# Performance work log

Measured on AMD Instinct MI355X. Metric: run time of the kernel, lower is better.

The kernel has to match this reference:

```python
import jax, jax.numpy as jnp
import numpy as np

NREF, NALT, B, D, F = 131072, 32768, 4096, 128, 512
H = F // 2  # d_ffn // 2
EPS = 1e-5


def _ln(x, w, b):
    m = jnp.mean(x, axis=-1, keepdims=True)
    v = jnp.mean((x - m) ** 2, axis=-1, keepdims=True)
    return (x - m) * jax.lax.rsqrt(v + EPS) * w + b


def setup_inputs() -> dict:
    key = jax.random.key(0)
    ks = jax.random.split(key, 16)
    s = 0.02
    return {
        "ref_flat": jax.random.normal(ks[0], (NREF, D), jnp.float32),
        "alt_flat": jax.random.normal(ks[1], (NALT, D), jnp.float32),
        "ref_seg": jnp.sort(jax.random.randint(ks[2], (NREF,), 0, B)),
        "alt_seg": jnp.sort(jax.random.randint(ks[3], (NALT,), 0, B)),
        "norm1_w": jnp.ones((D,), jnp.float32),
        "norm1_b": jnp.zeros((D,), jnp.float32),
        "w1_ref": jax.random.normal(ks[4], (D, F), jnp.float32) * s,
        "b1_ref": jnp.zeros((F,), jnp.float32),
        "w1_alt": jax.random.normal(ks[5], (D, F), jnp.float32) * s,
        "b1_alt": jnp.zeros((F,), jnp.float32),
        "norm2_w": jnp.ones((H,), jnp.float32),
        "norm2_b": jnp.zeros((H,), jnp.float32),
        "alpha_ref": jnp.float32(0.01),
        "alpha_alt": jnp.float32(0.01),
        "beta_ref": jnp.float32(0.01),
        "beta_alt": jnp.float32(0.01),
        "gamma": jnp.float32(0.01),
        "ref_regularizer": 0.1 * jnp.ones((H,), jnp.float32),
        "reg_w_pre": jnp.float32(np.log(0.1)),
        "w2_ref": jax.random.normal(ks[6], (H, D), jnp.float32) * s,
        "b2_ref": jnp.zeros((D,), jnp.float32),
        "w2_alt": jax.random.normal(ks[7], (H, D), jnp.float32) * s,
        "b2_alt": jnp.zeros((D,), jnp.float32),
    }


def reference(ref_flat, alt_flat, ref_seg, alt_seg,
              norm1_w, norm1_b, w1_ref, b1_ref, w1_alt, b1_alt,
              norm2_w, norm2_b, alpha_ref, alpha_alt, beta_ref, beta_alt,
              gamma, ref_regularizer, reg_w_pre, w2_ref, b2_ref, w2_alt, b2_alt):
    # proj1 + SELU on flattened ragged reads
    zr = jax.nn.selu(_ln(ref_flat, norm1_w, norm1_b) @ w1_ref + b1_ref)   # [NREF, F]
    za = jax.nn.selu(_ln(alt_flat, norm1_w, norm1_b) @ w1_alt + b1_alt)   # [NALT, F]
    z1r, z2r = zr[:, :H], zr[:, H:]
    z1a, z2a = za[:, :H], za[:, H:]
    z2r = _ln(z2r, norm2_w, norm2_b)
    z2a = _ln(z2a, norm2_w, norm2_b)

    cnt_r = jax.ops.segment_sum(jnp.ones((NREF,), z2r.dtype), ref_seg, num_segments=B)
    cnt_a = jax.ops.segment_sum(jnp.ones((NALT,), z2a.dtype), alt_seg, num_segments=B)
    reg_w = jnp.exp(reg_w_pre) + 0.25
    # regularized mean field over each ref set
    ref_mf = (jax.ops.segment_sum(z2r, ref_seg, num_segments=B)
              + reg_w * ref_regularizer) / (cnt_r[:, None] + reg_w)       # [B, H]
    alt_mf = jax.ops.segment_sum(z2a, alt_seg, num_segments=B) \
             / jnp.maximum(cnt_a, 1.0)[:, None]                            # [B, H]

    ref_gate = z2r * alpha_ref + 1.0 + (beta_ref * ref_mf)[ref_seg]
    alt_gate = z2a * alpha_alt + 1.0 + (beta_alt * alt_mf + gamma * ref_mf)[alt_seg]

    out_r = ref_flat + (z1r * ref_gate) @ w2_ref + b2_ref
    out_a = alt_flat + (z1a * alt_gate) @ w2_alt + b2_alt
    return out_r, out_a
```

## Files before the change

### kernel.cpp

```cpp
#include <hip/hip_runtime.h>
#include <hip/hip_bf16.h>

#define NREF 131072
#define NALT 32768
#define BSEG 4096
#define D 128
#define F 512
#define H 256
#define EPS 1e-5f

typedef short short8 __attribute__((ext_vector_type(8)));
typedef float f32x4 __attribute__((ext_vector_type(4)));

__device__ __forceinline__ float selu_f(float z) {
    const float sc = 1.0507009873554805f;
    const float al = 1.6732632423543772f;
    return z > 0.f ? sc * z : sc * al * (__expf(z) - 1.f);
}

__device__ __forceinline__ short f2bf(float v) {
    __bf16 b = (__bf16)v;
    return __builtin_bit_cast(short, b);
}

__device__ __forceinline__ float bf2f(short s) {
    return (float)__builtin_bit_cast(__bf16, s);
}

__global__ void pack_w(const float* __restrict__ w, __bf16* __restrict__ wp, int KT, int N) {
    int idx = blockIdx.x * 256 + threadIdx.x;
    int j = idx & 7;
    int l = (idx >> 3) & 63;
    int t = idx >> 9;
    int kt = t % KT;
    int nt = t / KT;
    int k = kt * 32 + ((l >> 4) << 3) + j;
    int n = (nt << 4) + (l & 15);
    wp[idx] = (__bf16)w[k * N + n];
}

__global__ __launch_bounds__(256, 4)
void pass1_kernel(const float* __restrict__ x, const int* __restrict__ seg,
                  const __bf16* __restrict__ w1p, const float* __restrict__ b1,
                  const float* __restrict__ n1w, const float* __restrict__ n1b,
                  const float* __restrict__ n2w, const float* __restrict__ n2b,
                  float* __restrict__ seg_sum, float* __restrict__ seg_cnt,
                  __bf16* __restrict__ z2n_out) {
    __shared__ __align__(16) __bf16 ys[32 * 128];
    __shared__ __align__(16) __bf16 z2s[32 * 256];
    __shared__ float n2w_s[H], n2b_s[H];
    __shared__ int seg_s[32];

    const int tid = threadIdx.x;
    const int lane = tid & 63;
    const int wv = tid >> 6;
    const int q = lane >> 4, m0 = lane & 15;
    const size_t row0 = (size_t)blockIdx.x * 32;

    short8 bb[2][4];
    #pragma unroll
    for (int p = 0; p < 2; ++p)
        #pragma unroll
        for (int kt = 0; kt < 4; ++kt)
            bb[p][kt] = *reinterpret_cast<const short8*>(
                w1p + ((size_t)((16 + wv * 4 + p) * 4 + kt) * 64 + lane) * 8);
    float b1v[4];
    #pragma unroll
    for (int nt = 0; nt < 4; ++nt) b1v[nt] = b1[256 + (wv * 4 + nt) * 16 + m0];

    const int r = tid >> 3, g = tid & 7;
    float xr[16];
    #pragma unroll
    for (int i = 0; i < 4; ++i) {
        float4 t = *reinterpret_cast<const float4*>(x + (row0 + r) * D + g * 16 + i * 4);
        xr[i * 4 + 0] = t.x; xr[i * 4 + 1] = t.y; xr[i * 4 + 2] = t.z; xr[i * 4 + 3] = t.w;
    }
    float w1r[16], c1r[16];
    #pragma unroll
    for (int i = 0; i < 4; ++i) {
        float4 t = *reinterpret_cast<const float4*>(n1w + g * 16 + i * 4);
        w1r[i * 4 + 0] = t.x; w1r[i * 4 + 1] = t.y; w1r[i * 4 + 2] = t.z; w1r[i * 4 + 3] = t.w;
        float4 u = *reinterpret_cast<const float4*>(n1b + g * 16 + i * 4);
        c1r[i * 4 + 0] = u.x; c1r[i * 4 + 1] = u.y; c1r[i * 4 + 2] = u.z; c1r[i * 4 + 3] = u.w;
    }

    n2w_s[tid] = n2w[tid]; n2b_s[tid] = n2b[tid];
    if (tid < 32) seg_s[tid] = seg[row0 + tid];

    {
        float s = 0.f, ss = 0.f;
        #pragma unroll
        for (int i = 0; i < 16; ++i) { s += xr[i]; ss += xr[i] * xr[i]; }
        s += __shfl_xor(s, 1); ss += __shfl_xor(ss, 1);
        s += __shfl_xor(s, 2); ss += __shfl_xor(ss, 2);
        s += __shfl_xor(s, 4); ss += __shfl_xor(ss, 4);
        float mean = s * (1.f / 128.f);
        float var = ss * (1.f / 128.f) - mean * mean;
        float rsv = rsqrtf(var + EPS);
        const int swr = (r & 7) << 3;
        #pragma unroll
        for (int h = 0; h < 2; ++h) {
            short8 pk;
            #pragma unroll
            for (int j = 0; j < 8; ++j)
                pk[j] = f2bf((xr[h * 8 + j] - mean) * rsv * w1r[h * 8 + j] + c1r[h * 8 + j]);
            *reinterpret_cast<short8*>(&ys[r * 128 + ((g * 16 + h * 8) ^ swr)]) = pk;
        }
    }
    __syncthreads();

    {
        const int swm = (m0 & 7) << 3;
        const int ccol = q << 3;
        short8 a0[4], a1[4];
        #pragma unroll
        for (int kt = 0; kt < 4; ++kt) {
            a0[kt] = *reinterpret_cast<const short8*>(&ys[m0 * 128 + ((kt * 32 + ccol) ^ swm)]);
            a1[kt] = *reinterpret_cast<const short8*>(&ys[(m0 + 16) * 128 + ((kt * 32 + ccol) ^ swm)]);
        }
        #pragma unroll
        for (int nt = 0; nt < 4; ++nt) {
            f32x4 acc0 = {0.f, 0.f, 0.f, 0.f};
            f32x4 acc1 = {0.f, 0.f, 0.f, 0.f};
            #pragma unroll
            for (int kt = 0; kt < 4; ++kt) {
                acc0 = __builtin_amdgcn_mfma_f32_16x16x32_bf16(a0[kt], bb[nt & 1][kt], acc0, 0, 0, 0);
                acc1 = __builtin_amdgcn_mfma_f32_16x16x32_bf16(a1[kt], bb[nt & 1][kt], acc1, 0, 0, 0);
            }
            if (nt < 2) {
                #pragma unroll
                for (int kt = 0; kt < 4; ++kt)
                    bb[nt & 1][kt] = *reinterpret_cast<const short8*>(
                        w1p + ((size_t)((16 + wv * 4 + nt + 2) * 4 + kt) * 64 + lane) * 8);
            }
            int cz = (wv * 4 + nt) * 16 + m0;
            #pragma unroll
            for (int reg = 0; reg < 4; ++reg) {
                int r0 = (q << 2) + reg;
                int r1 = r0 + 16;
                z2s[r0 * 256 + (cz ^ ((r0 & 7) << 3))] = (__bf16)selu_f(acc0[reg] + b1v[nt]);
                z2s[r1 * 256 + (cz ^ ((r1 & 7) << 3))] = (__bf16)selu_f(acc1[reg] + b1v[nt]);
            }
        }
    }
    __syncthreads();

    {
        const int swr = (r & 7) << 3;
        float vb[32];
        float s2 = 0.f, q2 = 0.f;
        #pragma unroll
        for (int i = 0; i < 4; ++i) {
            short8 v = *reinterpret_cast<const short8*>(&z2s[r * 256 + ((g * 32 + i * 8) ^ swr)]);
            #pragma unroll
            for (int j = 0; j < 8; ++j) {
                float f = bf2f(v[j]);
                vb[i * 8 + j] = f; s2 += f; q2 += f * f;
            }
        }
        s2 += __shfl_xor(s2, 1); q2 += __shfl_xor(q2, 1);
        s2 += __shfl_xor(s2, 2); q2 += __shfl_xor(q2, 2);
        s2 += __shfl_xor(s2, 4); q2 += __shfl_xor(q2, 4);
        float mean2 = s2 * (1.f / 256.f);
        float var2 = q2 * (1.f / 256.f) - mean2 * mean2;
        float rs2 = rsqrtf(var2 + EPS);
        #pragma unroll
        for (int i = 0; i < 4; ++i) {
            short8 o;
            #pragma unroll
            for (int j = 0; j < 8; ++j) {
                int col = g * 32 + i * 8 + j;
                o[j] = f2bf((vb[i * 8 + j] - mean2) * rs2 * n2w_s[col] + n2b_s[col]);
            }
            *reinterpret_cast<short8*>(&z2s[r * 256 + ((g * 32 + i * 8) ^ swr)]) = o;
            *reinterpret_cast<short8*>(z2n_out + (row0 + r) * H + g * 32 + i * 8) = o;
        }
    }
    __syncthreads();

    {
        int c = tid;
        int s_cur = seg_s[0];
        float run = 0.f;
        for (int rr = 0; rr < 32; ++rr) {
            int sg = seg_s[rr];
            if (sg != s_cur) {
                atomicAdd(&seg_sum[(size_t)s_cur * H + c], run);
                run = 0.f; s_cur = sg;
            }
            run += (float)z2s[rr * 256 + (c ^ ((rr & 7) << 3))];
        }
        atomicAdd(&seg_sum[(size_t)s_cur * H + c], run);
        if (tid == 0) {
            int sc = seg_s[0]; float rl = 0.f;
            for (int rr = 0; rr < 32; ++rr) {
                if (seg_s[rr] != sc) { atomicAdd(&seg_cnt[sc], rl); rl = 0.f; sc = seg_s[rr]; }
                rl += 1.f;
            }
            atomicAdd(&seg_cnt[sc], rl);
        }
    }
}

__global__ void mf_ref_kernel(const float* __restrict__ sum_r, const float* __restrict__ cnt_r,
                              const float* __restrict__ regz, const float* __restrict__ reg_w_pre,
                              const float* __restrict__ beta_ref, float* __restrict__ G_ref) {
    int s = blockIdx.x, c = threadIdx.x;
    size_t i = (size_t)s * H + c;
    float rw = __expf(reg_w_pre[0]) + 0.25f;
    float mfr = (sum_r[i] + rw * regz[c]) / (cnt_r[s] + rw);
    G_ref[i] = beta_ref[0] * mfr;
}

__global__ void mf_alt_kernel(const float* __restrict__ sum_r, const float* __restrict__ cnt_r,
                              const float* __restrict__ sum_a, const float* __restrict__ cnt_a,
                              const float* __restrict__ regz, const float* __restrict__ reg_w_pre,
                              const float* __restrict__ beta_alt, const float* __restrict__ gamma,
                              float* __restrict__ G_alt) {
    int s = blockIdx.x, c = threadIdx.x;
    size_t i = (size_t)s * H + c;
    float rw = __expf(reg_w_pre[0]) + 0.25f;
    float mfr = (sum_r[i] + rw * regz[c]) / (cnt_r[s] + rw);
    float mfa = sum_a[i] / fmaxf(cnt_a[s], 1.f);
    G_alt[i] = beta_alt[0] * mfa + gamma[0] * mfr;
}

__global__ __launch_bounds__(256, 4)
void pass2_kernel(const float* __restrict__ x, const int* __restrict__ seg,
                  const __bf16* __restrict__ w1p, const float* __restrict__ b1,
                  const __bf16* __restrict__ w2p, const float* __restrict__ b2,
                  const float* __restrict__ n1w, const float* __restrict__ n1b,
                  const float* __restrict__ alpha_p, const float* __restrict__ G,
                  const __bf16* __restrict__ z2n, float* __restrict__ out) {
    __shared__ __align__(16) __bf16 ys[32 * 128];
    __shared__ __align__(16) __bf16 zs[32 * 256];

    const int tid = threadIdx.x;
    const int lane = tid & 63;
    const int wv = tid >> 6;
    const int q = lane >> 4, m0 = lane & 15;
    const size_t row0 = (size_t)blockIdx.x * 32;
    const int r = tid >> 3, g = tid & 7;

    short8 bb[2][4];
    #pragma unroll
    for (int p = 0; p < 2; ++p)
        #pragma unroll
        for (int kt = 0; kt < 4; ++kt)
            bb[p][kt] = *reinterpret_cast<const short8*>(
                w1p + ((size_t)((wv * 4 + p) * 4 + kt) * 64 + lane) * 8);
    float b1v[4];
    #pragma unroll
    for (int nt = 0; nt < 4; ++nt) b1v[nt] = b1[(wv * 4 + nt) * 16 + m0];

    const int segi = seg[row0 + r];
    const float alpha = alpha_p[0];

    float xr[16];
    #pragma unroll
    for (int i = 0; i < 4; ++i) {
        float4 t = *reinterpret_cast<const float4*>(x + (row0 + r) * D + g * 16 + i * 4);
        xr[i * 4 + 0] = t.x; xr[i * 4 + 1] = t.y; xr[i * 4 + 2] = t.z; xr[i * 4 + 3] = t.w;
    }
    float w1r[16], c1r[16];
    #pragma unroll
    for (int i = 0; i < 4; ++i) {
        float4 t = *reinterpret_cast<const float4*>(n1w + g * 16 + i * 4);
        w1r[i * 4 + 0] = t.x; w1r[i * 4 + 1] = t.y; w1r[i * 4 + 2] = t.z; w1r[i * 4 + 3] = t.w;
        float4 u = *reinterpret_cast<const float4*>(n1b + g * 16 + i * 4);
        c1r[i * 4 + 0] = u.x; c1r[i * 4 + 1] = u.y; c1r[i * 4 + 2] = u.z; c1r[i * 4 + 3] = u.w;
    }

    {
        float s = 0.f, ss = 0.f;
        #pragma unroll
        for (int i = 0; i < 16; ++i) { s += xr[i]; ss += xr[i] * xr[i]; }
        s += __shfl_xor(s, 1); ss += __shfl_xor(ss, 1);
        s += __shfl_xor(s, 2); ss += __shfl_xor(ss, 2);
        s += __shfl_xor(s, 4); ss += __shfl_xor(ss, 4);
        float mean = s * (1.f / 128.f);
        float var = ss * (1.f / 128.f) - mean * mean;
        float rsv = rsqrtf(var + EPS);
        const int swr = (r & 7) << 3;
        #pragma unroll
        for (int h = 0; h < 2; ++h) {
            short8 pk;
            #pragma unroll
            for (int j = 0; j < 8; ++j)
                pk[j] = f2bf((xr[h * 8 + j] - mean) * rsv * w1r[h * 8 + j] + c1r[h * 8 + j]);
            *reinterpret_cast<short8*>(&ys[r * 128 + ((g * 16 + h * 8) ^ swr)]) = pk;
        }
    }
    __syncthreads();

    {
        const int swm = (m0 & 7) << 3;
        const int ccol = q << 3;
        short8 a0[4], a1[4];
        #pragma unroll
        for (int kt = 0; kt < 4; ++kt) {
            a0[kt] = *reinterpret_cast<const short8*>(&ys[m0 * 128 + ((kt * 32 + ccol) ^ swm)]);
            a1[kt] = *reinterpret_cast<const short8*>(&ys[(m0 + 16) * 128 + ((kt * 32 + ccol) ^ swm)]);
        }
        #pragma unroll
        for (int nt = 0; nt < 4; ++nt) {
            f32x4 acc0 = {0.f, 0.f, 0.f, 0.f};
            f32x4 acc1 = {0.f, 0.f, 0.f, 0.f};
            #pragma unroll
            for (int kt = 0; kt < 4; ++kt) {
                acc0 = __builtin_amdgcn_mfma_f32_16x16x32_bf16(a0[kt], bb[nt & 1][kt], acc0, 0, 0, 0);
                acc1 = __builtin_amdgcn_mfma_f32_16x16x32_bf16(a1[kt], bb[nt & 1][kt], acc1, 0, 0, 0);
            }
            if (nt < 2) {
                #pragma unroll
                for (int kt = 0; kt < 4; ++kt)
                    bb[nt & 1][kt] = *reinterpret_cast<const short8*>(
                        w1p + ((size_t)((wv * 4 + nt + 2) * 4 + kt) * 64 + lane) * 8);
            }
            int cz = (wv * 4 + nt) * 16 + m0;
            #pragma unroll
            for (int reg = 0; reg < 4; ++reg) {
                int r0 = (q << 2) + reg;
                int r1 = r0 + 16;
                zs[r0 * 256 + (cz ^ ((r0 & 7) << 3))] = (__bf16)selu_f(acc0[reg] + b1v[nt]);
                zs[r1 * 256 + (cz ^ ((r1 & 7) << 3))] = (__bf16)selu_f(acc1[reg] + b1v[nt]);
            }
        }
    }

    short8 zn[4];
    #pragma unroll
    for (int i = 0; i < 4; ++i)
        zn[i] = *reinterpret_cast<const short8*>(z2n + (row0 + r) * H + g * 32 + i * 8);
    float gvf[32];
    {
        const float* Gp = G + (size_t)segi * H + g * 32;
        #pragma unroll
        for (int i = 0; i < 8; ++i) {
            float4 t = *reinterpret_cast<const float4*>(Gp + i * 4);
            gvf[i * 4 + 0] = t.x; gvf[i * 4 + 1] = t.y; gvf[i * 4 + 2] = t.z; gvf[i * 4 + 3] = t.w;
        }
    }
    short8 b2f[2][8];
    #pragma unroll
    for (int p = 0; p < 2; ++p)
        #pragma unroll
        for (int kt = 0; kt < 8; ++kt)
            b2f[p][kt] = *reinterpret_cast<const short8*>(
                w2p + ((size_t)((wv * 2 + p) * 8 + kt) * 64 + lane) * 8);
    float b2v[2];
    #pragma unroll
    for (int p = 0; p < 2; ++p) b2v[p] = b2[(wv * 2 + p) * 16 + m0];
    __syncthreads();

    {
        const int swr = (r & 7) << 3;
        #pragma unroll
        for (int i = 0; i < 4; ++i) {
            int idx = r * 256 + ((g * 32 + i * 8) ^ swr);
            short8 v = *reinterpret_cast<const short8*>(&zs[idx]);
            short8 o;
            #pragma unroll
            for (int j = 0; j < 8; ++j) {
                float gate = bf2f(zn[i][j]) * alpha + 1.f + gvf[i * 8 + j];
                o[j] = f2bf(bf2f(v[j]) * gate);
            }
            *reinterpret_cast<short8*>(&zs[idx]) = o;
        }
    }
    float xres[16];
    #pragma unroll
    for (int p = 0; p < 2; ++p) {
        int col = (wv * 2 + p) * 16 + m0;
        #pragma unroll
        for (int reg = 0; reg < 4; ++reg) {
            int r0 = (q << 2) + reg;
            xres[p * 8 + reg]     = x[(row0 + r0) * D + col];
            xres[p * 8 + 4 + reg] = x[(row0 + r0 + 16) * D + col];
        }
    }
    __syncthreads();

    {
        const int swm = (m0 & 7) << 3;
        const int ccol = q << 3;
        f32x4 zero = {0.f, 0.f, 0.f, 0.f};
        f32x4 acc[2][2] = {{zero, zero}, {zero, zero}};
        #pragma unroll
        for (int kt = 0; kt < 8; ++kt) {
            short8 a0 = *reinterpret_cast<const short8*>(&zs[m0 * 256 + ((kt * 32 + ccol) ^ swm)]);
            short8 a1 = *reinterpret_cast<const short8*>(&zs[(m0 + 16) * 256 + ((kt * 32 + ccol) ^ swm)]);
            #pragma unroll
            for (int p = 0; p < 2; ++p) {
                acc[p][0] = __builtin_amdgcn_mfma_f32_16x16x32_bf16(a0, b2f[p][kt], acc[p][0], 0, 0, 0);
                acc[p][1] = __builtin_amdgcn_mfma_f32_16x16x32_bf16(a1, b2f[p][kt], acc[p][1], 0, 0, 0);
            }
        }
        #pragma unroll
        for (int p = 0; p < 2; ++p) {
            int col = (wv * 2 + p) * 16 + m0;
            #pragma unroll
            for (int reg = 0; reg < 4; ++reg) {
                int r0 = (q << 2) + reg;
                out[(row0 + r0) * D + col]      = acc[p][0][reg] + b2v[p] + xres[p * 8 + reg];
                out[(row0 + r0 + 16) * D + col] = acc[p][1][reg] + b2v[p] + xres[p * 8 + 4 + reg];
            }
        }
    }
}

extern "C" void kernel_launch(void* const* d_in, const int* in_sizes, int n_in,
                              void* d_out, int out_size, void* d_ws, size_t ws_size,
                              hipStream_t stream) {
    const float* ref_flat = (const float*)d_in[0];
    const float* alt_flat = (const float*)d_in[1];
    const int*   ref_seg  = (const int*)d_in[2];
    const int*   alt_seg  = (const int*)d_in[3];
    const float* norm1_w  = (const float*)d_in[4];
    const float* norm1_b  = (const float*)d_in[5];
    const float* w1_ref   = (const float*)d_in[6];
    const float* b1_ref   = (const float*)d_in[7];
    const float* w1_alt   = (const float*)d_in[8];
    const float* b1_alt   = (const float*)d_in[9];
    const float* norm2_w  = (const float*)d_in[10];
    const float* norm2_b  = (const float*)d_in[11];
    const float* alpha_ref = (const float*)d_in[12];
    const float* alpha_alt = (const float*)d_in[13];
    const float* beta_ref  = (const float*)d_in[14];
    const float* beta_alt  = (const float*)d_in[15];
    const float* gamma     = (const float*)d_in[16];
    const float* ref_regularizer = (const float*)d_in[17];
    const float* reg_w_pre = (const float*)d_in[18];
    const float* w2_ref   = (const float*)d_in[19];
    const float* b2_ref   = (const float*)d_in[20];
    const float* w2_alt   = (const float*)d_in[21];
    const float* b2_alt   = (const float*)d_in[22];

    char* ws = (char*)d_ws;
    float* sum_r = (float*)(ws);
    float* sum_a = (float*)(ws + 4194304);
    float* cnt_r = (float*)(ws + 8388608);
    float* cnt_a = (float*)(ws + 8404992);
    float* G_ref = (float*)(ws + 8421376);
    float* G_alt = (float*)(ws + 12615680);
    __bf16* w1p_r = (__bf16*)(ws + 16809984);
    __bf16* w1p_a = (__bf16*)(ws + 16941056);
    __bf16* w2p_r = (__bf16*)(ws + 17072128);
    __bf16* w2p_a = (__bf16*)(ws + 17137664);
    __bf16* z2nb  = (__bf16*)(ws + 17203200);

    hipMemsetAsync(d_ws, 0, 8421376, stream);

    pack_w<<<256, 256, 0, stream>>>(w1_ref, w1p_r, 4, F);
    pack_w<<<256, 256, 0, stream>>>(w1_alt, w1p_a, 4, F);
    pack_w<<<128, 256, 0, stream>>>(w2_ref, w2p_r, 8, D);
    pack_w<<<128, 256, 0, stream>>>(w2_alt, w2p_a, 8, D);

    pass1_kernel<<<NREF/32, 256, 0, stream>>>(ref_flat, ref_seg, w1p_r, b1_ref,
                                              norm1_w, norm1_b, norm2_w, norm2_b,
                                              sum_r, cnt_r, z2nb);
    mf_ref_kernel<<<BSEG, 256, 0, stream>>>(sum_r, cnt_r, ref_regularizer, reg_w_pre,
                                            beta_ref, G_ref);
    pass2_kernel<<<NREF/32, 256, 0, stream>>>(ref_flat, ref_seg, w1p_r, b1_ref, w2p_r, b2_ref,
                                              norm1_w, norm1_b, alpha_ref, G_ref, z2nb,
                                              (float*)d_out);

    pass1_kernel<<<NALT/32, 256, 0, stream>>>(alt_flat, alt_seg, w1p_a, b1_alt,
                                              norm1_w, norm1_b, norm2_w, norm2_b,
                                              sum_a, cnt_a, z2nb);
    mf_alt_kernel<<<BSEG, 256, 0, stream>>>(sum_r, cnt_r, sum_a, cnt_a,
                                            ref_regularizer, reg_w_pre,
                                            beta_alt, gamma, G_alt);
    pass2_kernel<<<NALT/32, 256, 0, stream>>>(alt_flat, alt_seg, w1p_a, b1_alt, w2p_a, b2_alt,
                                              norm1_w, norm1_b, alpha_alt, G_alt, z2nb,
                                              (float*)d_out + (size_t)NREF * D);
}
```

Before: 324.3 us.

## Merge ref and alt passes into single launches and fuse prep kernels

Weight packing and workspace zeroing are folded into one prep kernel, replacing a memset and four pack launches. The ref and alt pass1/pass2 launches are merged into single grids that pick the ref or alt branch by block index, and the two mean-field kernels become one. This cuts launch count and the tail idle time between the smaller alt launches. It needs a separate z2n buffer for alt, so it falls back to sequential launches when the workspace is too small.

```diff
diff --git a/kernel.cpp b/kernel.cpp
--- a/kernel.cpp
+++ b/kernel.cpp
@@ -8,6 +8,8 @@
 #define F 512
 #define H 256
 #define EPS 1e-5f
+#define NB_REF 4096
+#define NB_ALT 1024
 
 typedef short short8 __attribute__((ext_vector_type(8)));
 typedef float f32x4 __attribute__((ext_vector_type(4)));
@@ -27,35 +29,67 @@
     return (float)__builtin_bit_cast(__bf16, s);
 }
 
-__global__ void pack_w(const float* __restrict__ w, __bf16* __restrict__ wp, int KT, int N) {
-    int idx = blockIdx.x * 256 + threadIdx.x;
-    int j = idx & 7;
-    int l = (idx >> 3) & 63;
-    int t = idx >> 9;
-    int kt = t % KT;
-    int nt = t / KT;
-    int k = kt * 32 + ((l >> 4) << 3) + j;
-    int n = (nt << 4) + (l & 15);
-    wp[idx] = (__bf16)w[k * N + n];
+__global__ void prep_kernel(const float* __restrict__ w1_ref, const float* __restrict__ w1_alt,
+                            const float* __restrict__ w2_ref, const float* __restrict__ w2_alt,
+                            __bf16* __restrict__ w1p_r, __bf16* __restrict__ w1p_a,
+                            __bf16* __restrict__ w2p_r, __bf16* __restrict__ w2p_a,
+                            float* __restrict__ zbase) {
+    int b = blockIdx.x;
+    if (b < 768) {
+        const float* w; __bf16* wp; int KT, N, idx;
+        if (b < 256)      { w = w1_ref; wp = w1p_r; KT = 4; N = F; idx = b * 256 + threadIdx.x; }
+        else if (b < 512) { w = w1_alt; wp = w1p_a; KT = 4; N = F; idx = (b - 256) * 256 + threadIdx.x; }
+        else if (b < 640) { w = w2_ref; wp = w2p_r; KT = 8; N = D; idx = (b - 512) * 256 + threadIdx.x; }
+        else              { w = w2_alt; wp = w2p_a; KT = 8; N = D; idx = (b - 640) * 256 + threadIdx.x; }
+        int j = idx & 7;
+        int l = (idx >> 3) & 63;
+        int t = idx >> 9;
+        int kt = t % KT;
+        int nt = t / KT;
+        int k = kt * 32 + ((l >> 4) << 3) + j;
+        int n = (nt << 4) + (l & 15);
+        wp[idx] = (__bf16)w[k * N + n];
+    } else {
+        int t = (b - 768) * 256 + threadIdx.x;
+        float4 z = {0.f, 0.f, 0.f, 0.f};
+        for (int i = t; i < 526336; i += 512 * 256)
+            reinterpret_cast<float4*>(zbase)[i] = z;
+    }
 }
 
 __global__ __launch_bounds__(256, 4)
-void pass1_kernel(const float* __restrict__ x, const int* __restrict__ seg,
-                  const __bf16* __restrict__ w1p, const float* __restrict__ b1,
+void pass1_kernel(const float* __restrict__ xr_, const float* __restrict__ xa_,
+                  const int* __restrict__ segr_, const int* __restrict__ sega_,
+                  const __bf16* __restrict__ w1pr_, const __bf16* __restrict__ w1pa_,
+                  const float* __restrict__ b1r_, const float* __restrict__ b1a_,
                   const float* __restrict__ n1w, const float* __restrict__ n1b,
                   const float* __restrict__ n2w, const float* __restrict__ n2b,
-                  float* __restrict__ seg_sum, float* __restrict__ seg_cnt,
-                  __bf16* __restrict__ z2n_out) {
+                  float* __restrict__ sumr_, float* __restrict__ cntr_,
+                  float* __restrict__ suma_, float* __restrict__ cnta_,
+                  __bf16* __restrict__ z2nr_, __bf16* __restrict__ z2na_,
+                  int boff) {
     __shared__ __align__(16) __bf16 ys[32 * 128];
     __shared__ __align__(16) __bf16 z2s[32 * 256];
     __shared__ float n2w_s[H], n2b_s[H];
     __shared__ int seg_s[32];
 
+    const int b = blockIdx.x + boff;
+    const float* x; const int* seg; const __bf16* w1p; const float* b1;
+    float* seg_sum; float* seg_cnt; __bf16* z2n_out; size_t row0;
+    if (b < NB_REF) {
+        x = xr_; seg = segr_; w1p = w1pr_; b1 = b1r_;
+        seg_sum = sumr_; seg_cnt = cntr_; z2n_out = z2nr_;
+        row0 = (size_t)b * 32;
+    } else {
+        x = xa_; seg = sega_; w1p = w1pa_; b1 = b1a_;
+        seg_sum = suma_; seg_cnt = cnta_; z2n_out = z2na_;
+        row0 = (size_t)(b - NB_REF) * 32;
+    }
+
     const int tid = threadIdx.x;
     const int lane = tid & 63;
     const int wv = tid >> 6;
     const int q = lane >> 4, m0 = lane & 15;
-    const size_t row0 = (size_t)blockIdx.x * 32;
 
     short8 bb[2][4];
     #pragma unroll
@@ -202,44 +236,54 @@
     }
 }
 
-__global__ void mf_ref_kernel(const float* __restrict__ sum_r, const float* __restrict__ cnt_r,
-                              const float* __restrict__ regz, const float* __restrict__ reg_w_pre,
-                              const float* __restrict__ beta_ref, float* __restrict__ G_ref) {
-    int s = blockIdx.x, c = threadIdx.x;
-    size_t i = (size_t)s * H + c;
-    float rw = __expf(reg_w_pre[0]) + 0.25f;
-    float mfr = (sum_r[i] + rw * regz[c]) / (cnt_r[s] + rw);
-    G_ref[i] = beta_ref[0] * mfr;
-}
-
-__global__ void mf_alt_kernel(const float* __restrict__ sum_r, const float* __restrict__ cnt_r,
-                              const float* __restrict__ sum_a, const float* __restrict__ cnt_a,
-                              const float* __restrict__ regz, const float* __restrict__ reg_w_pre,
-                              const float* __restrict__ beta_alt, const float* __restrict__ gamma,
-                              float* __restrict__ G_alt) {
+__global__ void mf_kernel(const float* __restrict__ sum_r, const float* __restrict__ cnt_r,
+                          const float* __restrict__ sum_a, const float* __restrict__ cnt_a,
+                          const float* __restrict__ regz, const float* __restrict__ reg_w_pre,
+                          const float* __restrict__ beta_ref, const float* __restrict__ beta_alt,
+                          const float* __restrict__ gamma,
+                          float* __restrict__ G_ref, float* __restrict__ G_alt) {
     int s = blockIdx.x, c = threadIdx.x;
     size_t i = (size_t)s * H + c;
     float rw = __expf(reg_w_pre[0]) + 0.25f;
     float mfr = (sum_r[i] + rw * regz[c]) / (cnt_r[s] + rw);
     float mfa = sum_a[i] / fmaxf(cnt_a[s], 1.f);
+    G_ref[i] = beta_ref[0] * mfr;
     G_alt[i] = beta_alt[0] * mfa + gamma[0] * mfr;
 }
 
 __global__ __launch_bounds__(256, 4)
-void pass2_kernel(const float* __restrict__ x, const int* __restrict__ seg,
-                  const __bf16* __restrict__ w1p, const float* __restrict__ b1,
-                  const __bf16* __restrict__ w2p, const float* __restrict__ b2,
+void pass2_kernel(const float* __restrict__ xr_, const float* __restrict__ xa_,
+                  const int* __restrict__ segr_, const int* __restrict__ sega_,
+                  const __bf16* __restrict__ w1pr_, const __bf16* __restrict__ w1pa_,
+                  const float* __restrict__ b1r_, const float* __restrict__ b1a_,
+                  const __bf16* __restrict__ w2pr_, const __bf16* __restrict__ w2pa_,
+                  const float* __restrict__ b2r_, const float* __restrict__ b2a_,
                   const float* __restrict__ n1w, const float* __restrict__ n1b,
-                  const float* __restrict__ alpha_p, const float* __restrict__ G,
-                  const __bf16* __restrict__ z2n, float* __restrict__ out) {
+                  const float* __restrict__ alphar_, const float* __restrict__ alphaa_,
+                  const float* __restrict__ Gr_, const float* __restrict__ Ga_,
+                  const __bf16* __restrict__ z2nr_, const __bf16* __restrict__ z2na_,
+                  float* __restrict__ out_, int boff) {
     __shared__ __align__(16) __bf16 ys[32 * 128];
     __shared__ __align__(16) __bf16 zs[32 * 256];
+
+    const int b = blockIdx.x + boff;
+    const float* x; const int* seg; const __bf16* w1p; const float* b1;
+    const __bf16* w2p; const float* b2; const float* alpha_p; const float* G;
+    const __bf16* z2n; float* out; size_t row0;
+    if (b < NB_REF) {
+        x = xr_; seg = segr_; w1p = w1pr_; b1 = b1r_; w2p = w2pr_; b2 = b2r_;
+        alpha_p = alphar_; G = Gr_; z2n = z2nr_; out = out_;
+        row0 = (size_t)b * 32;
+    } else {
+        x = xa_; seg = sega_; w1p = w1pa_; b1 = b1a_; w2p = w2pa_; b2 = b2a_;
+        alpha_p = alphaa_; G = Ga_; z2n = z2na_; out = out_ + (size_t)NREF * D;
+        row0 = (size_t)(b - NB_REF) * 32;
+    }
 
     const int tid = threadIdx.x;
     const int lane = tid & 63;
     const int wv = tid >> 6;
     const int q = lane >> 4, m0 = lane & 15;
-    const size_t row0 = (size_t)blockIdx.x * 32;
     const int r = tid >> 3, g = tid & 7;
 
     short8 bb[2][4];
@@ -447,31 +491,49 @@
     __bf16* w1p_a = (__bf16*)(ws + 16941056);
     __bf16* w2p_r = (__bf16*)(ws + 17072128);
     __bf16* w2p_a = (__bf16*)(ws + 17137664);
-    __bf16* z2nb  = (__bf16*)(ws + 17203200);
-
-    hipMemsetAsync(d_ws, 0, 8421376, stream);
-
-    pack_w<<<256, 256, 0, stream>>>(w1_ref, w1p_r, 4, F);
-    pack_w<<<256, 256, 0, stream>>>(w1_alt, w1p_a, 4, F);
-    pack_w<<<128, 256, 0, stream>>>(w2_ref, w2p_r, 8, D);
-    pack_w<<<128, 256, 0, stream>>>(w2_alt, w2p_a, 8, D);
-
-    pass1_kernel<<<NREF/32, 256, 0, stream>>>(ref_flat, ref_seg, w1p_r, b1_ref,
-                                              norm1_w, norm1_b, norm2_w, norm2_b,
-                                              sum_r, cnt_r, z2nb);
-    mf_ref_kernel<<<BSEG, 256, 0, stream>>>(sum_r, cnt_r, ref_regularizer, reg_w_pre,
-                                            beta_ref, G_ref);
-    pass2_kernel<<<NREF/32, 256, 0, stream>>>(ref_flat, ref_seg, w1p_r, b1_ref, w2p_r, b2_ref,
-                                              norm1_w, norm1_b, alpha_ref, G_ref, z2nb,
-                                              (float*)d_out);
-
-    pass1_kernel<<<NALT/32, 256, 0, stream>>>(alt_flat, alt_seg, w1p_a, b1_alt,
-                                              norm1_w, norm1_b, norm2_w, norm2_b,
-                                              sum_a, cnt_a, z2nb);
-    mf_alt_kernel<<<BSEG, 256, 0, stream>>>(sum_r, cnt_r, sum_a, cnt_a,
+    __bf16* z2n_r = (__bf16*)(ws + 17203200);
+    __bf16* z2n_a = (__bf16*)(ws + 84312064);
+
+    const bool merged = ws_size >= (size_t)101089280;
+    if (!merged) z2n_a = z2n_r;
+
+    prep_kernel<<<1280, 256, 0, stream>>>(w1_ref, w1_alt, w2_ref, w2_alt,
+                                          w1p_r, w1p_a, w2p_r, w2p_a, (float*)ws);
+
+    if (merged) {
+        pass1_kernel<<<NB_REF + NB_ALT, 256, 0, stream>>>(
+            ref_flat, alt_flat, ref_seg, alt_seg, w1p_r, w1p_a, b1_ref, b1_alt,
+            norm1_w, norm1_b, norm2_w, norm2_b,
+            sum_r, cnt_r, sum_a, cnt_a, z2n_r, z2n_a, 0);
+        mf_kernel<<<BSEG, 256, 0, stream>>>(sum_r, cnt_r, sum_a, cnt_a,
                                             ref_regularizer, reg_w_pre,
-                                            beta_alt, gamma, G_alt);
-    pass2_kernel<<<NALT/32, 256, 0, stream>>>(alt_flat, alt_seg, w1p_a, b1_alt, w2p_a, b2_alt,
-                                              norm1_w, norm1_b, alpha_alt, G_alt, z2nb,
-                                              (float*)d_out + (size_t)NREF * D);
-}
+                                            beta_ref, beta_alt, gamma, G_ref, G_alt);
+        pass2_kernel<<<NB_REF + NB_ALT, 256, 0, stream>>>(
+            ref_flat, alt_flat, ref_seg, alt_seg, w1p_r, w1p_a, b1_ref, b1_alt,
+            w2p_r, w2p_a, b2_ref, b2_alt, norm1_w, norm1_b,
+            alpha_ref, alpha_alt, G_ref, G_alt, z2n_r, z2n_a, (float*)d_out, 0);
+    } else {
+        pass1_kernel<<<NB_REF, 256, 0, stream>>>(
+            ref_flat, alt_flat, ref_seg, alt_seg, w1p_r, w1p_a, b1_ref, b1_alt,
+            norm1_w, norm1_b, norm2_w, norm2_b,
+            sum_r, cnt_r, sum_a, cnt_a, z2n_r, z2n_a, 0);
+        mf_kernel<<<BSEG, 256, 0, stream>>>(sum_r, cnt_r, sum_a, cnt_a,
+                                            ref_regularizer, reg_w_pre,
+                                            beta_ref, beta_alt, gamma, G_ref, G_alt);
+        pass2_kernel<<<NB_REF, 256, 0, stream>>>(
+            ref_flat, alt_flat, ref_seg, alt_seg, w1p_r, w1p_a, b1_ref, b1_alt,
+            w2p_r, w2p_a, b2_ref, b2_alt, norm1_w, norm1_b,
+            alpha_ref, alpha_alt, G_ref, G_alt, z2n_r, z2n_a, (float*)d_out, 0);
+        pass1_kernel<<<NB_ALT, 256, 0, stream>>>(
+            ref_flat, alt_flat, ref_seg, alt_seg, w1p_r, w1p_a, b1_ref, b1_alt,
+            norm1_w, norm1_b, norm2_w, norm2_b,
+            sum_r, cnt_r, sum_a, cnt_a, z2n_r, z2n_a, NB_REF);
+        mf_kernel<<<BSEG, 256, 0, stream>>>(sum_r, cnt_r, sum_a, cnt_a,
+                                            ref_regularizer, reg_w_pre,
+                                            beta_ref, beta_alt, gamma, G_ref, G_alt);
+        pass2_kernel<<<NB_ALT, 256, 0, stream>>>(
+            ref_flat, alt_flat, ref_seg, alt_seg, w1p_r, w1p_a, b1_ref, b1_alt,
+            w2p_r, w2p_a, b2_ref, b2_alt, norm1_w, norm1_b,
+            alpha_ref, alpha_alt, G_ref, G_alt, z2n_r, z2n_a, (float*)d_out, NB_REF);
+    }
+}
```

Result: faster. 300.3 us (-7.4%).
